# Optimization experiments

Hardware: AMD Instinct MI355X
Metric: run time of the kernel (lower is better)

## Reference

```python
import math
import jax, jax.numpy as jnp
import numpy as np

B, S, D, H, DFF, MEM = 4, 1024, 1024, 16, 4096, 256
HD = D // H  # 64
EPS = 1e-5


def _ln(x, g, b):
    mu = jnp.mean(x, axis=-1, keepdims=True)
    var = jnp.mean(jnp.square(x - mu), axis=-1, keepdims=True)
    return (x - mu) * jax.lax.rsqrt(var + EPS) * g + b


def _rope(x, cos, sin):
    # x: (b, h, s, hd); cos/sin: (>=s, hd//2)
    s = x.shape[2]
    xp = x.reshape(*x.shape[:-1], -1, 2)
    x0, x1 = xp[..., 0], xp[..., 1]
    c = cos[:s][None, None]
    sn = sin[:s][None, None]
    r0 = x0 * c - x1 * sn
    r1 = x0 * sn + x1 * c
    return jnp.stack([r0, r1], axis=-1).reshape(x.shape)


def setup_inputs() -> dict:
    key = jax.random.key(0)
    ks = jax.random.split(key, 16)
    p = lambda k, shape: jax.random.normal(k, shape, dtype=jnp.float32) * 0.02

    tgt = jax.random.normal(ks[0], (B, S, D), dtype=jnp.float32)
    memory = jax.random.normal(ks[1], (B, MEM, D), dtype=jnp.float32)

    # causal additive mask (s, s)
    tgt_mask = jnp.where(jnp.tril(jnp.ones((S, S), bool)), 0.0, -1e9).astype(jnp.float32)

    # RoPE freqs, theta=10000
    inv_freq = 1.0 / (10000.0 ** (np.arange(0, HD, 2, dtype=np.float32) / HD))
    ang = np.arange(S, dtype=np.float32)[:, None] * inv_freq[None, :]
    rope_cos = jnp.asarray(np.cos(ang))
    rope_sin = jnp.asarray(np.sin(ang))

    return {
        "tgt": tgt, "memory": memory, "tgt_mask": tgt_mask,
        "rope_cos": rope_cos, "rope_sin": rope_sin,
        "qkv_w": p(ks[2], (3 * D, D)), "qkv_b": jnp.zeros((3 * D,), jnp.float32),
        "out_w": p(ks[3], (D, D)), "out_b": jnp.zeros((D,), jnp.float32),
        "ca_in_w": p(ks[4], (3 * D, D)), "ca_in_b": jnp.zeros((3 * D,), jnp.float32),
        "ca_out_w": p(ks[5], (D, D)), "ca_out_b": jnp.zeros((D,), jnp.float32),
        "ffn_w1": p(ks[6], (DFF, D)), "ffn_b1": jnp.zeros((DFF,), jnp.float32),
        "ffn_w2": p(ks[7], (D, DFF)), "ffn_b2": jnp.zeros((D,), jnp.float32),
        "ln1_g": jnp.ones((D,), jnp.float32), "ln1_b": jnp.zeros((D,), jnp.float32),
        "ln2_g": jnp.ones((D,), jnp.float32), "ln2_b": jnp.zeros((D,), jnp.float32),
        "ln3_g": jnp.ones((D,), jnp.float32), "ln3_b": jnp.zeros((D,), jnp.float32),
    }


def reference(tgt, memory, tgt_mask, rope_cos, rope_sin,
              qkv_w, qkv_b, out_w, out_b,
              ca_in_w, ca_in_b, ca_out_w, ca_out_b,
              ffn_w1, ffn_b1, ffn_w2, ffn_b2,
              ln1_g, ln1_b, ln2_g, ln2_b, ln3_g, ln3_b):
    b, s, d = tgt.shape
    scale = 1.0 / math.sqrt(HD)

    # ---- self-attention with RoPE ----
    x = _ln(tgt, ln1_g, ln1_b)
    qkv = (x @ qkv_w.T + qkv_b).reshape(b, s, 3, H, HD)
    qkv = jnp.transpose(qkv, (2, 0, 3, 1, 4))  # (3, b, h, s, hd)
    q, k, v = qkv[0], qkv[1], qkv[2]
    q = _rope(q, rope_cos, rope_sin)
    k = _rope(k, rope_cos, rope_sin)
    attn = jnp.einsum('bhqd,bhkd->bhqk', q, k) * scale
    attn = attn + tgt_mask[None, None]
    attn = jax.nn.softmax(attn, axis=-1)
    sa = jnp.einsum('bhqk,bhkd->bhqd', attn, v)
    sa = jnp.transpose(sa, (0, 2, 1, 3)).reshape(b, s, d)
    tgt = tgt + (sa @ out_w.T + out_b)

    # ---- cross-attention (standard MHA, no positional encoding) ----
    x = _ln(tgt, ln2_g, ln2_b)
    wq, wk, wv = jnp.split(ca_in_w, 3, axis=0)
    bq, bk, bv = jnp.split(ca_in_b, 3, axis=0)
    m = memory.shape[1]
    cq = (x @ wq.T + bq).reshape(b, s, H, HD).transpose(0, 2, 1, 3)
    ck = (memory @ wk.T + bk).reshape(b, m, H, HD).transpose(0, 2, 1, 3)
    cv = (memory @ wv.T + bv).reshape(b, m, H, HD).transpose(0, 2, 1, 3)
    cattn = jax.nn.softmax(jnp.einsum('bhqd,bhkd->bhqk', cq, ck) * scale, axis=-1)
    co = jnp.einsum('bhqk,bhkd->bhqd', cattn, cv)
    co = jnp.transpose(co, (0, 2, 1, 3)).reshape(b, s, d)
    tgt = tgt + (co @ ca_out_w.T + ca_out_b)

    # ---- FFN (exact GELU, as torch nn.GELU default) ----
    x = _ln(tgt, ln3_g, ln3_b)
    ff = jax.nn.gelu(x @ ffn_w1.T + ffn_b1, approximate=False) @ ffn_w2.T + ffn_b2
    return tgt + ff
```

## Files before the change

### kernel.cpp

```cpp
#include <hip/hip_runtime.h>
#include <hip/hip_bf16.h>


using bf16 = __hip_bfloat16;
typedef __bf16 bf16x8 __attribute__((ext_vector_type(8)));
typedef float f32x4 __attribute__((ext_vector_type(4)));

static constexpr int Bn = 4, Ssz = 1024, Dm = 1024, Hh = 16, HDd = 64, DFFn = 4096, MEMn = 256;

__device__ inline float bf2f(bf16 x) { return __bfloat162float(x); }
__device__ inline bf16 f2bf(float x) { return __float2bfloat16(x); }

__device__ __forceinline__ void gload16(const bf16* g, bf16* l) {
  __builtin_amdgcn_global_load_lds(
      (const __attribute__((address_space(1))) void*)g,
      (__attribute__((address_space(3))) void*)l, 16, 0, 0);
}

__global__ void detect_kernel(const unsigned* __restrict__ cosw, int* __restrict__ flag) {
  if (threadIdx.x == 0) *flag = (cosw[0] == 0x3F800000u) ? 1 : 0;
}

struct CanonArgs {
  const void* src[23];
  void* dst[23];
  int n[23];
};
__global__ __launch_bounds__(256) void canon_all(CanonArgs a, float* __restrict__ resid,
                                                 const int* __restrict__ flagp) {
  const int seg = blockIdx.y;
  const int n4 = a.n[seg] >> 2;
  if (n4 == 0) return;
  const int fl = *flagp;
  if (fl) {
    const float4* s = (const float4*)a.src[seg];
    bf16* d = (bf16*)a.dst[seg];
    for (int i = blockIdx.x * 256 + threadIdx.x; i < n4; i += gridDim.x * 256) {
      float4 v = s[i];
      bf16 t[4] = {f2bf(v.x), f2bf(v.y), f2bf(v.z), f2bf(v.w)};
      *reinterpret_cast<unsigned long long*>(d + i * 4) =
          *reinterpret_cast<unsigned long long*>(t);
      if (seg == 0) *reinterpret_cast<float4*>(resid + i * 4) = v;
    }
  } else {
    const unsigned long long* s = (const unsigned long long*)a.src[seg];
    unsigned long long* d = (unsigned long long*)a.dst[seg];
    for (int i = blockIdx.x * 256 + threadIdx.x; i < n4; i += gridDim.x * 256) {
      unsigned long long v = s[i];
      d[i] = v;
      if (seg == 0) {
        const unsigned short* u = reinterpret_cast<const unsigned short*>(&v);
        float4 f;
        f.x = __uint_as_float(((unsigned)u[0]) << 16);
        f.y = __uint_as_float(((unsigned)u[1]) << 16);
        f.z = __uint_as_float(((unsigned)u[2]) << 16);
        f.w = __uint_as_float(((unsigned)u[3]) << 16);
        *reinterpret_cast<float4*>(resid + i * 4) = f;
      }
    }
  }
}

__global__ __launch_bounds__(256) void ln_kernel(const float* __restrict__ x,
                                                 const bf16* __restrict__ g,
                                                 const bf16* __restrict__ bb,
                                                 bf16* __restrict__ y) {
  const int row = blockIdx.x;
  const float* xr = x + (size_t)row * Dm;
  const int i0 = threadIdx.x * 4;
  float4 v = *reinterpret_cast<const float4*>(xr + i0);
  float s = v.x + v.y + v.z + v.w;
  float ss = v.x * v.x + v.y * v.y + v.z * v.z + v.w * v.w;
#pragma unroll
  for (int o = 32; o > 0; o >>= 1) {
    s += __shfl_down(s, o);
    ss += __shfl_down(ss, o);
  }
  __shared__ float shs[4], shss[4];
  const int wave = threadIdx.x >> 6, lane = threadIdx.x & 63;
  if (lane == 0) { shs[wave] = s; shss[wave] = ss; }
  __syncthreads();
  s = shs[0] + shs[1] + shs[2] + shs[3];
  ss = shss[0] + shss[1] + shss[2] + shss[3];
  const float mu = s * (1.0f / Dm);
  const float var = fmaxf(ss * (1.0f / Dm) - mu * mu, 0.0f);
  const float rs = rsqrtf(var + 1e-5f);
  bf16* yr = y + (size_t)row * Dm + i0;
  float vv[4] = {v.x, v.y, v.z, v.w};
#pragma unroll
  for (int j = 0; j < 4; ++j)
    yr[j] = f2bf((vv[j] - mu) * rs * bf2f(g[i0 + j]) + bf2f(bb[i0 + j]));
}

__global__ __launch_bounds__(256) void gemm_bt(
    const bf16* __restrict__ A, const bf16* __restrict__ W,
    const bf16* __restrict__ bias, bf16* __restrict__ outB, float* __restrict__ outF,
    const float* __restrict__ residIn, float* __restrict__ residOut,
    const int* __restrict__ flagp, int M, int N, int K, int epi) {
  __shared__ bf16 As[64][40];
  __shared__ bf16 Ws[64][40];
  const int tid = threadIdx.x;
  const int m0 = blockIdx.x * 64, n0 = blockIdx.y * 64;
  const int wave = tid >> 6, lane = tid & 63;
  const int wm = wave >> 1, wn = wave & 1;
  const int quad = lane >> 4, m16 = lane & 15;
  const int lr = tid >> 2, lc = (tid & 3) * 8;

  f32x4 acc[2][2] = {};

  const bf16* Ap = A + (size_t)(m0 + lr) * K + lc;
  const bf16* Wp = W + (size_t)(n0 + lr) * K + lc;
  for (int k0 = 0; k0 < K; k0 += 32) {
    float4 av = *reinterpret_cast<const float4*>(Ap + k0);
    float4 wv = *reinterpret_cast<const float4*>(Wp + k0);
    *reinterpret_cast<float4*>(&As[lr][lc]) = av;
    *reinterpret_cast<float4*>(&Ws[lr][lc]) = wv;
    __syncthreads();
    bf16x8 aF[2], bF[2];
#pragma unroll
    for (int t = 0; t < 2; ++t) {
      aF[t] = *reinterpret_cast<const bf16x8*>(&As[wm * 32 + t * 16 + m16][quad * 8]);
      bF[t] = *reinterpret_cast<const bf16x8*>(&Ws[wn * 32 + t * 16 + m16][quad * 8]);
    }
#pragma unroll
    for (int mt = 0; mt < 2; ++mt)
#pragma unroll
      for (int nt = 0; nt < 2; ++nt)
        acc[mt][nt] = __builtin_amdgcn_mfma_f32_16x16x32_bf16(aF[mt], bF[nt], acc[mt][nt], 0, 0, 0);
    __syncthreads();
  }
  const int fl = (epi == 3) ? *flagp : 0;
#pragma unroll
  for (int mt = 0; mt < 2; ++mt) {
#pragma unroll
    for (int nt = 0; nt < 2; ++nt) {
      const int col = n0 + wn * 32 + nt * 16 + m16;
      const float bv = bf2f(bias[col]);
#pragma unroll
      for (int r = 0; r < 4; ++r) {
        const int row = m0 + wm * 32 + mt * 16 + quad * 4 + r;
        const size_t idx = (size_t)row * N + col;
        float v = acc[mt][nt][r] + bv;
        if (epi == 0) {
          outB[idx] = f2bf(v);
        } else if (epi == 1) {
          outB[idx] = f2bf(0.5f * v * (1.0f + erff(v * 0.70710678118654752f)));
        } else if (epi == 2) {
          residOut[idx] = residIn[idx] + v;
        } else {
          const float rr = residIn[idx] + v;
          if (fl) outF[idx] = rr; else outB[idx] = f2bf(rr);
        }
      }
    }
  }
}

__global__ __launch_bounds__(512) void gemm128(
    const bf16* __restrict__ A, const bf16* __restrict__ W,
    const bf16* __restrict__ bias, bf16* __restrict__ outB, float* __restrict__ outF,
    const float* __restrict__ residIn, float* __restrict__ residOut,
    const int* __restrict__ flagp, int M, int N, int K, int epi) {
  __shared__ bf16 As[4][128][32];
  __shared__ bf16 Ws[4][128][32];
  const int tid = threadIdx.x;
  const int wave = tid >> 6, lane = tid & 63;
  const int wm = wave >> 1;
  const int wn = wave & 1;
  const int quad = lane >> 4, m16 = lane & 15;
  const int m0 = blockIdx.x * 128, n0 = blockIdx.y * 128;

  const int sr = tid >> 2;
  const int sc = (tid & 3) * 8;
  const bf16* Ap = A + (size_t)(m0 + sr) * K + sc;
  const bf16* Wp = W + (size_t)(n0 + sr) * K + sc;

  f32x4 acc[2][4] = {};

#define STAGE128(T, BUF)                                   \
  {                                                        \
    const int kk_ = (T) * 32;                              \
    gload16(Ap + kk_, &As[BUF][sr][sc]);                   \
    gload16(Wp + kk_, &Ws[BUF][sr][sc]);                   \
  }

#define READS128(RB)                                                                        \
  _Pragma("unroll") for (int tt = 0; tt < 2; ++tt)                                          \
    aF[tt] = *reinterpret_cast<const bf16x8*>(&As[RB][wm * 32 + tt * 16 + m16][quad * 8]);  \
  _Pragma("unroll") for (int nt = 0; nt < 4; ++nt)                                          \
    bF[nt] = *reinterpret_cast<const bf16x8*>(&Ws[RB][wn * 64 + nt * 16 + m16][quad * 8]);

#define MFMAS128                                                                            \
  _Pragma("unroll") for (int mt = 0; mt < 2; ++mt)                                          \
  _Pragma("unroll") for (int nt = 0; nt < 4; ++nt)                                          \
    acc[mt][nt] = __builtin_amdgcn_mfma_f32_16x16x32_bf16(aF[mt], bF[nt], acc[mt][nt], 0, 0, 0);

  const int nsteps = K >> 5;
  STAGE128(0, 0)
  STAGE128(1, 1)
  STAGE128(2, 2)

  int rb = 0, sb = 3;
  for (int t = 0; t < nsteps - 2; ++t) {
    asm volatile("s_waitcnt vmcnt(4)" ::: "memory");
    __builtin_amdgcn_s_barrier();
    __builtin_amdgcn_sched_barrier(0);
    bf16x8 aF[2], bF[4];
    READS128(rb)
    __builtin_amdgcn_sched_barrier(0);
    if (t + 3 < nsteps) { STAGE128(t + 3, sb) }
    __builtin_amdgcn_sched_barrier(0);
    MFMAS128
    rb = (rb + 1 == 4) ? 0 : rb + 1;
    sb = (sb + 1 == 4) ? 0 : sb + 1;
  }
  {
    asm volatile("s_waitcnt vmcnt(2)" ::: "memory");
    __builtin_amdgcn_s_barrier();
    __builtin_amdgcn_sched_barrier(0);
    bf16x8 aF[2], bF[4];
    READS128(rb)
    MFMAS128
    rb = (rb + 1 == 4) ? 0 : rb + 1;
  }
  {
    asm volatile("s_waitcnt vmcnt(0)" ::: "memory");
    __builtin_amdgcn_s_barrier();
    __builtin_amdgcn_sched_barrier(0);
    bf16x8 aF[2], bF[4];
    READS128(rb)
    MFMAS128
  }
#undef STAGE128
#undef READS128
#undef MFMAS128

  const int fl = (epi == 3) ? *flagp : 0;
#pragma unroll
  for (int mt = 0; mt < 2; ++mt) {
#pragma unroll
    for (int nt = 0; nt < 4; ++nt) {
      const int col = n0 + wn * 64 + nt * 16 + m16;
      const float bv = bf2f(bias[col]);
#pragma unroll
      for (int r = 0; r < 4; ++r) {
        const int row = m0 + wm * 32 + mt * 16 + quad * 4 + r;
        const size_t idx = (size_t)row * N + col;
        float v = acc[mt][nt][r] + bv;
        if (epi == 0) {
          outB[idx] = f2bf(v);
        } else if (epi == 1) {
          outB[idx] = f2bf(0.5f * v * (1.0f + erff(v * 0.70710678118654752f)));
        } else if (epi == 2) {
          residOut[idx] = residIn[idx] + v;
        } else {
          const float rr = residIn[idx] + v;
          if (fl) outF[idx] = rr; else outB[idx] = f2bf(rr);
        }
      }
    }
  }
}

__global__ __launch_bounds__(512) void gemm256(
    const bf16* __restrict__ A, const bf16* __restrict__ W,
    const bf16* __restrict__ bias, bf16* __restrict__ outB,
    int M, int N, int K, int epi) {
  __shared__ bf16 Abuf[2][256 * 64];
  __shared__ bf16 Bbuf[2][256 * 64];
  const int tid = threadIdx.x;
  const int wave = tid >> 6, lane = tid & 63;
  const int wm = wave >> 2, wn = wave & 3;
  const int quad = lane >> 4, m16 = lane & 15;
  const int m0 = blockIdx.x * 256, n0 = blockIdx.y * 256;
  const int lr8 = lane >> 3, lc8 = lane & 7;
  const int gch = (lc8 ^ lr8) * 8;
  const int swz = m16 & 7;

  f32x4 acc[8][4] = {};

#define STAGE256(T, BUF)                                                         \
  { const int kb_ = (T) * 64 + gch;                                              \
    _Pragma("unroll") for (int i = 0; i < 4; ++i) {                              \
      const int rr = (wave * 4 + i) * 8 + lr8;                                   \
      gload16(A + (size_t)(m0 + rr) * K + kb_, &Abuf[BUF][rr * 64 + lc8 * 8]);   \
      gload16(W + (size_t)(n0 + rr) * K + kb_, &Bbuf[BUF][rr * 64 + lc8 * 8]);   \
    } }

  const int nsteps = K >> 6;
  STAGE256(0, 0)
  for (int t = 0; t < nsteps; ++t) {
    asm volatile("s_waitcnt vmcnt(0)" ::: "memory");
    __builtin_amdgcn_s_barrier();
    __builtin_amdgcn_sched_barrier(0);
    const int rb = t & 1;
    bf16x8 aF[2][8], bF[2][4];
#pragma unroll
    for (int kk = 0; kk < 2; ++kk) {
      const int cswz = ((quad + 4 * kk) ^ swz) * 8;
#pragma unroll
      for (int tt = 0; tt < 8; ++tt)
        aF[kk][tt] = *reinterpret_cast<const bf16x8*>(
            &Abuf[rb][(wm * 128 + tt * 16 + m16) * 64 + cswz]);
#pragma unroll
      for (int nt = 0; nt < 4; ++nt)
        bF[kk][nt] = *reinterpret_cast<const bf16x8*>(
            &Bbuf[rb][(wn * 64 + nt * 16 + m16) * 64 + cswz]);
    }
    __builtin_amdgcn_sched_barrier(0);
    if (t + 1 < nsteps) { STAGE256(t + 1, rb ^ 1) }
    __builtin_amdgcn_sched_barrier(0);
#pragma unroll
    for (int kk = 0; kk < 2; ++kk)
#pragma unroll
      for (int mt = 0; mt < 8; ++mt)
#pragma unroll
        for (int nt = 0; nt < 4; ++nt)
          acc[mt][nt] = __builtin_amdgcn_mfma_f32_16x16x32_bf16(
              aF[kk][mt], bF[kk][nt], acc[mt][nt], 0, 0, 0);
  }
#undef STAGE256

#pragma unroll
  for (int mt = 0; mt < 8; ++mt) {
#pragma unroll
    for (int nt = 0; nt < 4; ++nt) {
      const int col = n0 + wn * 64 + nt * 16 + m16;
      const float bv = bf2f(bias[col]);
#pragma unroll
      for (int r = 0; r < 4; ++r) {
        const int row = m0 + wm * 128 + mt * 16 + quad * 4 + r;
        const size_t idx = (size_t)row * N + col;
        float v = acc[mt][nt][r] + bv;
        outB[idx] = (epi == 1)
                        ? f2bf(0.5f * v * (1.0f + erff(v * 0.70710678118654752f)))
                        : f2bf(v);
      }
    }
  }
}

__global__ __launch_bounds__(256) void rope_kernel(bf16* __restrict__ qkv,
                                                   const bf16* __restrict__ cosb,
                                                   const bf16* __restrict__ sinb) {
  const int idx = blockIdx.x * 256 + threadIdx.x;
  const int i = idx & 31;
  const int h = (idx >> 5) & 15;
  const int r = idx >> 9;
  const int s = r & (Ssz - 1);
  const float c = bf2f(cosb[s * 32 + i]);
  const float sn = bf2f(sinb[s * 32 + i]);
  bf16* base = qkv + (size_t)r * (3 * Dm) + h * 64 + 2 * i;
  float x0 = bf2f(base[0]), x1 = bf2f(base[1]);
  base[0] = f2bf(x0 * c - x1 * sn);
  base[1] = f2bf(x0 * sn + x1 * c);
  x0 = bf2f(base[Dm]); x1 = bf2f(base[Dm + 1]);
  base[Dm] = f2bf(x0 * c - x1 * sn);
  base[Dm + 1] = f2bf(x0 * sn + x1 * c);
}

__global__ __launch_bounds__(512) void attn_mfma(
    const bf16* __restrict__ Qb, const bf16* __restrict__ Kb, const bf16* __restrict__ Vb,
    bf16* __restrict__ Ob, int qStride, int kvStride, int kvLen, int causal, float scale) {
  __shared__ bf16 Ks[64][72];
  __shared__ bf16 Vt[64][72];
  __shared__ bf16 Ps[128][72];
  const int tid = threadIdx.x;
  const int wave = tid >> 6, lane = tid & 63;
  const int quad = lane >> 4, m16 = lane & 15;
  const int b = blockIdx.z, h = blockIdx.y;

  for (int half = 0; half < 2; ++half) {
    const int qidx = (half == 0) ? blockIdx.x : (2 * gridDim.x - 1 - blockIdx.x);
    const int q0 = qidx * 128;
    __syncthreads();
    {
      const int sr = tid >> 2, sc = (tid & 3) * 16;
      const bf16* qp = Qb + (size_t)(b * Ssz + q0 + sr) * qStride + h * 64 + sc;
      float4 a = reinterpret_cast<const float4*>(qp)[0];
      float4 bb2 = reinterpret_cast<const float4*>(qp)[1];
      *reinterpret_cast<float4*>(&Ps[sr][sc]) = a;
      *reinterpret_cast<float4*>(&Ps[sr][sc + 8]) = bb2;
    }
    __syncthreads();
    bf16x8 qf[2];
    qf[0] = *reinterpret_cast<const bf16x8*>(&Ps[wave * 16 + m16][quad * 8]);
    qf[1] = *reinterpret_cast<const bf16x8*>(&Ps[wave * 16 + m16][32 + quad * 8]);

    f32x4 oacc[4] = {};
    float mrow[4], lrow[4];
#pragma unroll
    for (int r = 0; r < 4; ++r) { mrow[r] = -30000.0f; lrow[r] = 0.0f; }

    const int wrow0 = q0 + wave * 16;
    const int nk = causal ? (q0 + 128) : kvLen;
    for (int kt = 0; kt < nk; kt += 64) {
      {
        const int dbase = wave * 8;
        const bf16* kp = Kb + (size_t)(b * kvLen + kt + lane) * kvStride + h * 64 + dbase;
        float4 k1 = *reinterpret_cast<const float4*>(kp);
        *reinterpret_cast<float4*>(&Ks[lane][dbase]) = k1;
        const bf16* vp = Vb + (size_t)(b * kvLen + kt + lane) * kvStride + h * 64 + dbase;
        float4 v1 = *reinterpret_cast<const float4*>(vp);
        const bf16* tv = reinterpret_cast<const bf16*>(&v1);
#pragma unroll
        for (int j = 0; j < 8; ++j) Vt[dbase + j][lane] = tv[j];
      }
      __syncthreads();

      const bool live = (causal == 0) || (kt <= wrow0 + 15);
      if (live) {
        f32x4 sacc[4] = {};
#pragma unroll
        for (int nt = 0; nt < 4; ++nt) {
          bf16x8 kf0 = *reinterpret_cast<const bf16x8*>(&Ks[nt * 16 + m16][quad * 8]);
          bf16x8 kf1 = *reinterpret_cast<const bf16x8*>(&Ks[nt * 16 + m16][32 + quad * 8]);
          sacc[nt] = __builtin_amdgcn_mfma_f32_16x16x32_bf16(qf[0], kf0, sacc[nt], 0, 0, 0);
          sacc[nt] = __builtin_amdgcn_mfma_f32_16x16x32_bf16(qf[1], kf1, sacc[nt], 0, 0, 0);
        }
        const bool dmask = (causal != 0) && (kt + 63 > wrow0);
#pragma unroll
        for (int nt = 0; nt < 4; ++nt) {
#pragma unroll
          for (int r = 0; r < 4; ++r) {
            float s = sacc[nt][r] * scale;
            if (dmask && (kt + nt * 16 + m16 > wrow0 + quad * 4 + r)) s = -30000.0f;
            sacc[nt][r] = s;
          }
        }

#pragma unroll
        for (int r = 0; r < 4; ++r) {
          float mx = fmaxf(fmaxf(sacc[0][r], sacc[1][r]), fmaxf(sacc[2][r], sacc[3][r]));
#pragma unroll
          for (int off = 1; off < 16; off <<= 1) mx = fmaxf(mx, __shfl_xor(mx, off));
          const float mn = fmaxf(mrow[r], mx);
          const float corr = __expf(mrow[r] - mn);
          mrow[r] = mn;
          float psum = 0.0f;
#pragma unroll
          for (int nt = 0; nt < 4; ++nt) {
            const float p = __expf(sacc[nt][r] - mn);
            sacc[nt][r] = p;
            psum += p;
          }
#pragma unroll
          for (int off = 1; off < 16; off <<= 1) psum += __shfl_xor(psum, off);
          lrow[r] = lrow[r] * corr + psum;
#pragma unroll
          for (int nt = 0; nt < 4; ++nt) oacc[nt][r] *= corr;
#pragma unroll
          for (int nt = 0; nt < 4; ++nt)
            Ps[wave * 16 + quad * 4 + r][nt * 16 + m16] = f2bf(sacc[nt][r]);
        }
        bf16x8 pf0 = *reinterpret_cast<const bf16x8*>(&Ps[wave * 16 + m16][quad * 8]);
        bf16x8 pf1 = *reinterpret_cast<const bf16x8*>(&Ps[wave * 16 + m16][32 + quad * 8]);
#pragma unroll
        for (int nt = 0; nt < 4; ++nt) {
          bf16x8 vf0 = *reinterpret_cast<const bf16x8*>(&Vt[nt * 16 + m16][quad * 8]);
          bf16x8 vf1 = *reinterpret_cast<const bf16x8*>(&Vt[nt * 16 + m16][32 + quad * 8]);
          oacc[nt] = __builtin_amdgcn_mfma_f32_16x16x32_bf16(pf0, vf0, oacc[nt], 0, 0, 0);
          oacc[nt] = __builtin_amdgcn_mfma_f32_16x16x32_bf16(pf1, vf1, oacc[nt], 0, 0, 0);
        }
      }
      __syncthreads();
    }

    float inv[4];
#pragma unroll
    for (int r = 0; r < 4; ++r) inv[r] = 1.0f / lrow[r];
#pragma unroll
    for (int r = 0; r < 4; ++r) {
      bf16* op = Ob + (size_t)(b * Ssz + q0 + wave * 16 + quad * 4 + r) * Dm + h * 64 + m16;
#pragma unroll
      for (int nt = 0; nt < 4; ++nt) op[nt * 16] = f2bf(oacc[nt][r] * inv[r]);
    }
  }
}

extern "C" void kernel_launch(void* const* d_in, const int* in_sizes, int n_in,
                              void* d_out, int out_size, void* d_ws, size_t ws_size,
                              hipStream_t stream) {
  char* ws = (char*)d_ws;
  int* flagp   = (int*)ws;
  float* resid = (float*)(ws + (1ull << 20));
  bf16* xln    = (bf16*)(ws + (17ull << 20));
  bf16* aout   = (bf16*)(ws + (25ull << 20));
  bf16* big    = (bf16*)(ws + (33ull << 20));
  size_t off   = (65ull << 20);

  detect_kernel<<<1, 64, 0, stream>>>((const unsigned*)d_in[3], flagp);

  CanonArgs ca;
  bf16* c[23];
  for (int i = 0; i < 23; ++i) {
    if (i == 2) { c[i] = nullptr; ca.src[i] = d_in[i]; ca.dst[i] = nullptr; ca.n[i] = 0; continue; }
    c[i] = (bf16*)(ws + off);
    const int n = in_sizes[i];
    off += ((size_t)n * 2 + 255) & ~(size_t)255;
    ca.src[i] = d_in[i];
    ca.dst[i] = c[i];
    ca.n[i] = n;
  }
  canon_all<<<dim3(256, 23), 256, 0, stream>>>(ca, resid, flagp);

  const bf16 *memory = c[1], *rope_cos = c[3], *rope_sin = c[4];
  const bf16 *qkv_w = c[5], *qkv_b = c[6], *out_w = c[7], *out_b = c[8];
  const bf16 *ca_in_w = c[9], *ca_in_b = c[10], *ca_out_w = c[11], *ca_out_b = c[12];
  const bf16 *ffn_w1 = c[13], *ffn_b1 = c[14], *ffn_w2 = c[15], *ffn_b2 = c[16];
  const bf16 *ln1_g = c[17], *ln1_b = c[18], *ln2_g = c[19], *ln2_b = c[20];
  const bf16 *ln3_g = c[21], *ln3_b = c[22];

  bf16* qb = big;
  bf16* kb = (bf16*)(ws + (41ull << 20));
  bf16* vb = (bf16*)(ws + (43ull << 20));
  bf16* outB = (bf16*)d_out;
  float* outF = (float*)d_out;

  const int ROWS = Bn * Ssz;
  const float scale = 0.125f;

  ln_kernel<<<ROWS, 256, 0, stream>>>(resid, ln1_g, ln1_b, xln);
  gemm256<<<dim3(ROWS / 256, (3 * Dm) / 256), 512, 0, stream>>>(
      xln, qkv_w, qkv_b, big, ROWS, 3 * Dm, Dm, 0);
  rope_kernel<<<(ROWS * Hh * (HDd / 2)) / 256, 256, 0, stream>>>(big, rope_cos, rope_sin);
  attn_mfma<<<dim3(Ssz / 256, Hh, Bn), 512, 0, stream>>>(
      big, big + Dm, big + 2 * Dm, aout, 3 * Dm, 3 * Dm, Ssz, 1, scale);
  gemm128<<<dim3(ROWS / 128, Dm / 128), 512, 0, stream>>>(
      aout, out_w, out_b, nullptr, nullptr, resid, resid, nullptr, ROWS, Dm, Dm, 2);

  ln_kernel<<<ROWS, 256, 0, stream>>>(resid, ln2_g, ln2_b, xln);
  gemm128<<<dim3(ROWS / 128, Dm / 128), 512, 0, stream>>>(
      xln, ca_in_w, ca_in_b, qb, nullptr, nullptr, nullptr, nullptr, ROWS, Dm, Dm, 0);
  gemm_bt<<<dim3((Bn * MEMn) / 64, Dm / 64), 256, 0, stream>>>(
      memory, ca_in_w + (size_t)Dm * Dm, ca_in_b + Dm, kb, nullptr, nullptr, nullptr, nullptr,
      Bn * MEMn, Dm, Dm, 0);
  gemm_bt<<<dim3((Bn * MEMn) / 64, Dm / 64), 256, 0, stream>>>(
      memory, ca_in_w + (size_t)2 * Dm * Dm, ca_in_b + 2 * Dm, vb, nullptr, nullptr, nullptr, nullptr,
      Bn * MEMn, Dm, Dm, 0);
  attn_mfma<<<dim3(Ssz / 256, Hh, Bn), 512, 0, stream>>>(
      qb, kb, vb, aout, Dm, Dm, MEMn, 0, scale);
  gemm128<<<dim3(ROWS / 128, Dm / 128), 512, 0, stream>>>(
      aout, ca_out_w, ca_out_b, nullptr, nullptr, resid, resid, nullptr, ROWS, Dm, Dm, 2);

  ln_kernel<<<ROWS, 256, 0, stream>>>(resid, ln3_g, ln3_b, xln);
  gemm256<<<dim3(ROWS / 256, DFFn / 256), 512, 0, stream>>>(
      xln, ffn_w1, ffn_b1, big, ROWS, DFFn, Dm, 1);
  gemm128<<<dim3(ROWS / 128, Dm / 128), 512, 0, stream>>>(
      big, ffn_w2, ffn_b2, outB, outF, resid, nullptr, flagp, ROWS, Dm, DFFn, 3);
}
```

Measured before the change: 507.2 us.

## Restructure gemm128 to double-buffered BK=64 swizzled tiles and issue prefetch before LDS reads

gemm128 drops its 4-stage BK=32 ring buffer for a 2-stage BK=64 double buffer. The LDS layout is XOR-swizzled to avoid bank conflicts, and each k-step now does two MFMA k-slices. Both gemm kernels now issue the next tile's global-to-LDS loads before reading the current tile from LDS, so the fetch is in flight earlier. This halves the number of barriers per K in gemm128. The cost is a shallower prefetch depth (one tile ahead, waiting with vmcnt(0)), which may expose memory latency.

```diff
diff --git a/kernel.cpp b/kernel.cpp
--- a/kernel.cpp
+++ b/kernel.cpp
@@ -161,8 +161,8 @@
     const bf16* __restrict__ bias, bf16* __restrict__ outB, float* __restrict__ outF,
     const float* __restrict__ residIn, float* __restrict__ residOut,
     const int* __restrict__ flagp, int M, int N, int K, int epi) {
-  __shared__ bf16 As[4][128][32];
-  __shared__ bf16 Ws[4][128][32];
+  __shared__ bf16 As[2][128][64];
+  __shared__ bf16 Ws[2][128][64];
   const int tid = threadIdx.x;
   const int wave = tid >> 6, lane = tid & 63;
   const int wm = wave >> 1;
@@ -170,65 +170,54 @@
   const int quad = lane >> 4, m16 = lane & 15;
   const int m0 = blockIdx.x * 128, n0 = blockIdx.y * 128;
 
-  const int sr = tid >> 2;
-  const int sc = (tid & 3) * 8;
-  const bf16* Ap = A + (size_t)(m0 + sr) * K + sc;
-  const bf16* Wp = W + (size_t)(n0 + sr) * K + sc;
+  const int srow = tid >> 3;
+  const int gch = ((tid & 7) ^ ((tid >> 3) & 7));
+  const bf16* Ap0 = A + (size_t)(m0 + srow) * K + gch * 8;
+  const bf16* Ap1 = A + (size_t)(m0 + 64 + srow) * K + gch * 8;
+  const bf16* Wp0 = W + (size_t)(n0 + srow) * K + gch * 8;
+  const bf16* Wp1 = W + (size_t)(n0 + 64 + srow) * K + gch * 8;
+  const int swz = m16 & 7;
 
   f32x4 acc[2][4] = {};
 
-#define STAGE128(T, BUF)                                   \
-  {                                                        \
-    const int kk_ = (T) * 32;                              \
-    gload16(Ap + kk_, &As[BUF][sr][sc]);                   \
-    gload16(Wp + kk_, &Ws[BUF][sr][sc]);                   \
-  }
-
-#define READS128(RB)                                                                        \
-  _Pragma("unroll") for (int tt = 0; tt < 2; ++tt)                                          \
-    aF[tt] = *reinterpret_cast<const bf16x8*>(&As[RB][wm * 32 + tt * 16 + m16][quad * 8]);  \
-  _Pragma("unroll") for (int nt = 0; nt < 4; ++nt)                                          \
-    bF[nt] = *reinterpret_cast<const bf16x8*>(&Ws[RB][wn * 64 + nt * 16 + m16][quad * 8]);
+#define STAGE128(T, BUF)                                               \
+  {                                                                    \
+    const int kk_ = (T) * 64;                                          \
+    bf16* ab = &As[BUF][0][0];                                         \
+    bf16* wb = &Ws[BUF][0][0];                                         \
+    gload16(Ap0 + kk_, ab + tid * 8);                                  \
+    gload16(Ap1 + kk_, ab + 4096 + tid * 8);                           \
+    gload16(Wp0 + kk_, wb + tid * 8);                                  \
+    gload16(Wp1 + kk_, wb + 4096 + tid * 8);                           \
+  }
+
+#define READS128(RB)                                                                       \
+  _Pragma("unroll") for (int ks = 0; ks < 2; ++ks) {                                       \
+    const int pc_ = ((quad + 4 * ks) ^ swz) * 8;                                           \
+    _Pragma("unroll") for (int tt = 0; tt < 2; ++tt)                                       \
+      aF[ks][tt] = *reinterpret_cast<const bf16x8*>(&As[RB][wm * 32 + tt * 16 + m16][pc_]); \
+    _Pragma("unroll") for (int nt = 0; nt < 4; ++nt)                                       \
+      bF[ks][nt] = *reinterpret_cast<const bf16x8*>(&Ws[RB][wn * 64 + nt * 16 + m16][pc_]); \
+  }
 
 #define MFMAS128                                                                            \
+  _Pragma("unroll") for (int ks = 0; ks < 2; ++ks)                                          \
   _Pragma("unroll") for (int mt = 0; mt < 2; ++mt)                                          \
   _Pragma("unroll") for (int nt = 0; nt < 4; ++nt)                                          \
-    acc[mt][nt] = __builtin_amdgcn_mfma_f32_16x16x32_bf16(aF[mt], bF[nt], acc[mt][nt], 0, 0, 0);
-
-  const int nsteps = K >> 5;
+    acc[mt][nt] = __builtin_amdgcn_mfma_f32_16x16x32_bf16(aF[ks][mt], bF[ks][nt], acc[mt][nt], 0, 0, 0);
+
+  const int nsteps = K >> 6;
   STAGE128(0, 0)
-  STAGE128(1, 1)
-  STAGE128(2, 2)
-
-  int rb = 0, sb = 3;
-  for (int t = 0; t < nsteps - 2; ++t) {
-    asm volatile("s_waitcnt vmcnt(4)" ::: "memory");
-    __builtin_amdgcn_s_barrier();
-    __builtin_amdgcn_sched_barrier(0);
-    bf16x8 aF[2], bF[4];
-    READS128(rb)
-    __builtin_amdgcn_sched_barrier(0);
-    if (t + 3 < nsteps) { STAGE128(t + 3, sb) }
-    __builtin_amdgcn_sched_barrier(0);
-    MFMAS128
-    rb = (rb + 1 == 4) ? 0 : rb + 1;
-    sb = (sb + 1 == 4) ? 0 : sb + 1;
-  }
-  {
-    asm volatile("s_waitcnt vmcnt(2)" ::: "memory");
-    __builtin_amdgcn_s_barrier();
-    __builtin_amdgcn_sched_barrier(0);
-    bf16x8 aF[2], bF[4];
-    READS128(rb)
-    MFMAS128
-    rb = (rb + 1 == 4) ? 0 : rb + 1;
-  }
-  {
+  for (int t = 0; t < nsteps; ++t) {
     asm volatile("s_waitcnt vmcnt(0)" ::: "memory");
     __builtin_amdgcn_s_barrier();
     __builtin_amdgcn_sched_barrier(0);
-    bf16x8 aF[2], bF[4];
+    const int rb = t & 1;
+    if (t + 1 < nsteps) { STAGE128(t + 1, rb ^ 1) }
+    __builtin_amdgcn_sched_barrier(0);
+    bf16x8 aF[2][2], bF[2][4];
     READS128(rb)
+    __builtin_amdgcn_sched_barrier(0);
     MFMAS128
   }
 #undef STAGE128
@@ -294,6 +283,8 @@
     __builtin_amdgcn_s_barrier();
     __builtin_amdgcn_sched_barrier(0);
     const int rb = t & 1;
+    if (t + 1 < nsteps) { STAGE256(t + 1, rb ^ 1) }
+    __builtin_amdgcn_sched_barrier(0);
     bf16x8 aF[2][8], bF[2][4];
 #pragma unroll
     for (int kk = 0; kk < 2; ++kk) {
@@ -307,8 +298,6 @@
         bF[kk][nt] = *reinterpret_cast<const bf16x8*>(
             &Bbuf[rb][(wn * 64 + nt * 16 + m16) * 64 + cswz]);
     }
-    __builtin_amdgcn_sched_barrier(0);
-    if (t + 1 < nsteps) { STAGE256(t + 1, rb ^ 1) }
     __builtin_amdgcn_sched_barrier(0);
 #pragma unroll
     for (int kk = 0; kk < 2; ++kk)
```

Measured after the change: 544.3 us. 1.07x slower.
